# Performance work log

Hardware: AMD Instinct MI355X
Metric: run time of the kernel (lower is better)

## Reference

```python
import jax, jax.numpy as jnp
import numpy as np

GROUPS = 8
EPS = 1e-3  # keras GroupNormalization default epsilon


def group_norm(x, gamma, beta):
    # x: [B,H,W,C], groups over channel axis
    B, H, W, C = x.shape
    g = GROUPS
    xr = x.reshape(B, H, W, g, C // g)
    mean = jnp.mean(xr, axis=(1, 2, 4), keepdims=True)
    var = jnp.var(xr, axis=(1, 2, 4), keepdims=True)
    xn = (xr - mean) * jax.lax.rsqrt(var + EPS)
    xn = xn.reshape(B, H, W, C)
    return xn * gamma + beta


def setup_inputs() -> dict:
    key = jax.random.key(0)
    ks = jax.random.split(key, 6)
    B, H, W, C = 8, 64, 64, 64
    std = 0.02
    return {
        "x": jax.random.normal(ks[0], (B, H, W, C), dtype=jnp.float32),
        "gamma": jnp.ones((C,), dtype=jnp.float32),
        "beta": jnp.zeros((C,), dtype=jnp.float32),
        "wq": jax.random.normal(ks[1], (C, C), dtype=jnp.float32) * std,
        "bq": jnp.zeros((C,), dtype=jnp.float32),
        "wk": jax.random.normal(ks[2], (C, C), dtype=jnp.float32) * std,
        "bk": jnp.zeros((C,), dtype=jnp.float32),
        "wv": jax.random.normal(ks[3], (C, C), dtype=jnp.float32) * std,
        "bv": jnp.zeros((C,), dtype=jnp.float32),
        "wp": jax.random.normal(ks[4], (C, C), dtype=jnp.float32) * std,
        "bp": jnp.zeros((C,), dtype=jnp.float32),
    }


def reference(x, gamma, beta, wq, bq, wk, bk, wv, bv, wp, bp):
    B, H, W, C = x.shape
    scale = jnp.asarray(C, x.dtype) ** -0.5
    h = group_norm(x, gamma, beta)  # note: residual uses normalized input (as in source)
    q = h @ wq + bq
    k = h @ wk + bk
    v = h @ wv + bv
    # full O((HW)^2) score tensor, exactly as the original
    attn = jnp.einsum('bhwc,bHWc->bhwHW', q, k) * scale
    attn = jax.nn.softmax(attn.reshape(B, H, W, H * W), axis=-1)
    attn = attn.reshape(B, H, W, H, W)
    proj = jnp.einsum('bhwHW,bHWc->bhwc', attn, v)
    proj = proj @ wp + bp
    return h + proj
```

## Files before the change

### kernel.cpp

```cpp
#include <hip/hip_runtime.h>

#define NTOK 4096
#define CH 64
#define LOG2E 1.4426950408889634f

typedef __bf16 bf8 __attribute__((ext_vector_type(8)));
typedef __bf16 bf4 __attribute__((ext_vector_type(4)));
typedef _Float16 h8 __attribute__((ext_vector_type(8)));
typedef _Float16 h4 __attribute__((ext_vector_type(4)));
typedef float f4 __attribute__((ext_vector_type(4)));

__device__ __forceinline__ f4 mfma16(bf8 a, bf8 b, f4 c) {
    return __builtin_amdgcn_mfma_f32_16x16x32_bf16(a, b, c, 0, 0, 0);
}
__device__ __forceinline__ f4 mfma32h(h8 a, h8 b, f4 c) {
    return __builtin_amdgcn_mfma_f32_16x16x32_f16(a, b, c, 0, 0, 0);
}

__global__ __launch_bounds__(256) void pre_kernel(const float* __restrict__ wq,
                                                  const float* __restrict__ wk,
                                                  const float* __restrict__ wv,
                                                  const float* __restrict__ wp,
                                                  const float* __restrict__ x,
                                                  __bf16* __restrict__ wqt,
                                                  __bf16* __restrict__ wkt,
                                                  __bf16* __restrict__ wvt,
                                                  __bf16* __restrict__ wpt,
                                                  float* __restrict__ gpart) {
    int t = threadIdx.x;
    if (blockIdx.x < 4) {
        int m = blockIdx.x;
        const float* src = (m == 0) ? wq : (m == 1) ? wk : (m == 2) ? wv : wp;
        __bf16* dst      = (m == 0) ? wqt : (m == 1) ? wkt : (m == 2) ? wvt : wpt;
        __shared__ float s[64][65];
        for (int i = 0; i < 16; ++i) {
            int e = i * 256 + t;
            s[e >> 6][e & 63] = src[e];
        }
        __syncthreads();
        int o = t >> 2, seg = t & 3;
        for (int j = 0; j < 16; ++j) {
            int in = seg * 16 + j;
            dst[o * 64 + in] = (__bf16)s[in][o];
        }
        return;
    }
    int bid = blockIdx.x - 4;
    int b = bid >> 6, slab = bid & 63;
    const float4* xb = (const float4*)(x + (size_t)(b * NTOK + slab * 64) * CH);
    float s = 0.f, ss = 0.f;
    for (int i = 0; i < 4; ++i) {
        int row = (t >> 4) + i * 16;
        float4 v = xb[row * 16 + (t & 15)];
        s  += v.x + v.y + v.z + v.w;
        ss += v.x * v.x + v.y * v.y + v.z * v.z + v.w * v.w;
    }
    __shared__ float ls[256], lss[256];
    ls[t] = s; lss[t] = ss;
    __syncthreads();
    if (t < 8) {
        float a = 0.f, aa = 0.f;
        for (int p = 0; p < 16; ++p) {
            a  += ls[p * 16 + 2 * t]  + ls[p * 16 + 2 * t + 1];
            aa += lss[p * 16 + 2 * t] + lss[p * 16 + 2 * t + 1];
        }
        gpart[((b * 64 + slab) * 8 + t) * 2 + 0] = a;
        gpart[((b * 64 + slab) * 8 + t) * 2 + 1] = aa;
    }
}

__global__ __launch_bounds__(256) void qkv_gn(const float* __restrict__ x,
                                              const float* __restrict__ gpart,
                                              const float* __restrict__ gamma,
                                              const float* __restrict__ beta,
                                              const __bf16* __restrict__ wqt,
                                              const __bf16* __restrict__ wkt,
                                              const __bf16* __restrict__ wvt,
                                              const float* __restrict__ bq,
                                              const float* __restrict__ bk,
                                              const float* __restrict__ bv,
                                              __bf16* __restrict__ q,
                                              __bf16* __restrict__ k,
                                              _Float16* __restrict__ vT) {
    __shared__ __bf16 W[3][64][72];
    __shared__ __bf16 Hl[64][72];
    __shared__ _Float16 Vst[64][68];
    __shared__ float red[128];
    __shared__ float sstat[16];
    int t = threadIdx.x;
    size_t rowbase = (size_t)blockIdx.x * 64;
    int b = (int)(rowbase >> 12), tokbase = (int)(rowbase & 4095);
    if (t < 64) {
        int gi = t & 7, c = t >> 3;
        const float2* gp = (const float2*)gpart + (size_t)b * 512 + gi;
        float a = 0.f, aa = 0.f;
        for (int p = c * 8; p < c * 8 + 8; ++p) {
            float2 v = gp[(size_t)p * 8];
            a += v.x; aa += v.y;
        }
        red[t * 2] = a; red[t * 2 + 1] = aa;
    }
    for (int m = 0; m < 3; ++m) {
        const __bf16* src = (m == 0) ? wqt : (m == 1) ? wkt : wvt;
        for (int i = 0; i < 2; ++i) {
            int e = i * 256 + t, row = e >> 3, ch = e & 7;
            *(bf8*)&W[m][row][ch * 8] = *(const bf8*)(src + row * 64 + ch * 8);
        }
    }
    __syncthreads();
    if (t < 8) {
        float a = 0.f, aa = 0.f;
        for (int c = 0; c < 8; ++c) {
            a  += red[(c * 8 + t) * 2];
            aa += red[(c * 8 + t) * 2 + 1];
        }
        float mean = a * (1.f / 32768.f);
        float var = aa * (1.f / 32768.f) - mean * mean;
        sstat[t * 2 + 0] = mean;
        sstat[t * 2 + 1] = rsqrtf(var + 1e-3f);
    }
    __syncthreads();
    {
        int c4 = (t & 15) * 4, grp = c4 >> 3;
        float mean = sstat[grp * 2], rstd = sstat[grp * 2 + 1];
        float g0 = gamma[c4] * rstd, g1 = gamma[c4 + 1] * rstd,
              g2 = gamma[c4 + 2] * rstd, g3 = gamma[c4 + 3] * rstd;
        float b0 = beta[c4], b1 = beta[c4 + 1], b2 = beta[c4 + 2], b3 = beta[c4 + 3];
        const float4* xb = (const float4*)(x + rowbase * 64);
        for (int i = 0; i < 4; ++i) {
            int row = (t >> 4) + i * 16;
            float4 v = xb[row * 16 + (t & 15)];
            bf4 hv;
            hv[0] = (__bf16)((v.x - mean) * g0 + b0);
            hv[1] = (__bf16)((v.y - mean) * g1 + b1);
            hv[2] = (__bf16)((v.z - mean) * g2 + b2);
            hv[3] = (__bf16)((v.w - mean) * g3 + b3);
            *(bf4*)&Hl[row][c4] = hv;
        }
    }
    __syncthreads();
    int lane = t & 63, wave = t >> 6, quad = lane >> 4, l15 = lane & 15;
    bf8 a0 = *(const bf8*)&Hl[wave * 16 + l15][quad * 8];
    bf8 a1 = *(const bf8*)&Hl[wave * 16 + l15][32 + quad * 8];
    for (int m = 0; m < 3; ++m) {
        const float* bias = (m == 0) ? bq : (m == 1) ? bk : bv;
        float sc = (m == 0) ? 0.125f * LOG2E : 1.0f;
        for (int tt = 0; tt < 4; ++tt) {
            int col = l15 + 16 * tt;
            bf8 b0 = *(const bf8*)&W[m][col][quad * 8];
            bf8 b1 = *(const bf8*)&W[m][col][32 + quad * 8];
            f4 acc = {0.f, 0.f, 0.f, 0.f};
            acc = mfma16(a0, b0, acc);
            acc = mfma16(a1, b1, acc);
            float bb = bias[col];
            if (m == 2) {
                for (int r = 0; r < 4; ++r)
                    Vst[col][wave * 16 + quad * 4 + r] = (_Float16)(acc[r] + bb);
            } else {
                __bf16* dst = (m == 0) ? q : k;
                for (int r = 0; r < 4; ++r) {
                    float val = (acc[r] + bb) * sc;
                    dst[(rowbase + wave * 16 + quad * 4 + r) * 64 + col] = (__bf16)val;
                }
            }
        }
    }
    __syncthreads();
    {
        int d = wave * 16 + l15;
        for (int kb = 0; kb < 2; ++kb) {
            h4 lo = *(const h4*)&Vst[d][kb * 32 + quad * 4];
            h4 hi = *(const h4*)&Vst[d][kb * 32 + 16 + quad * 4];
            h8 o;
            o[0] = lo[0]; o[1] = lo[1]; o[2] = lo[2]; o[3] = lo[3];
            o[4] = hi[0]; o[5] = hi[1]; o[6] = hi[2]; o[7] = hi[3];
            _Float16* dst = vT + ((((size_t)b * 128 + (tokbase >> 5) + kb) * 4 + wave) * 64
                                  + lane) * 8;
            *(h8*)dst = o;
        }
    }
}

__global__ __launch_bounds__(256, 2) void attn_final(const __bf16* __restrict__ q,
                                                     const __bf16* __restrict__ k,
                                                     const _Float16* __restrict__ vt,
                                                     const __bf16* __restrict__ wpt,
                                                     const float* __restrict__ bp,
                                                     const float* __restrict__ x,
                                                     const float* __restrict__ gpart,
                                                     const float* __restrict__ gamma,
                                                     const float* __restrict__ beta,
                                                     float* __restrict__ out) {
    __shared__ _Float16 Om[2][64][72];
    __shared__ float sS[2][64];
    __shared__ __bf16 Wl[64][72];
    __shared__ __bf16 Ol[64][72];
    __shared__ float red[128];
    __shared__ float sstat[16], sg[64], sb[64];

    int bid = blockIdx.x;
    int qt = bid >> 3, b = bid & 7;
    int t = threadIdx.x, lane = t & 63, w = t >> 6, quad = lane >> 4, l15 = lane & 15;

    for (int i = 0; i < 2; ++i) {
        int e = i * 256 + t, row = e >> 3, ch = e & 7;
        *(bf8*)&Wl[row][ch * 8] = *(const bf8*)(wpt + row * 64 + ch * 8);
    }
    if (t < 64) { sg[t] = gamma[t]; sb[t] = beta[t]; }
    if (t < 64) {
        int gi = t & 7, c = t >> 3;
        const float2* gp = (const float2*)gpart + (size_t)b * 512 + gi;
        float a = 0.f, aa = 0.f;
        for (int p = c * 8; p < c * 8 + 8; ++p) {
            float2 v = gp[(size_t)p * 8];
            a += v.x; aa += v.y;
        }
        red[t * 2] = a; red[t * 2 + 1] = aa;
    }

    const __bf16* qbase = q + ((size_t)b * NTOK + qt * 64) * 64;
    bf8 aq[4][2];
    for (int s = 0; s < 4; ++s) {
        const __bf16* r = qbase + (s * 16 + l15) * 64;
        aq[s][0] = *(const bf8*)(r + quad * 8);
        aq[s][1] = *(const bf8*)(r + 32 + quad * 8);
    }
    const __bf16* kbase   = k  + ((size_t)b * NTOK + w * 1024) * 64;
    const _Float16* vbase = vt + (size_t)b * 262144 + (size_t)(w * 32) * 2048 + lane * 8;

    f4 acc[4][4] = {};
    float li[4] = {0.f, 0.f, 0.f, 0.f};

    for (int it = 0; it < 32; ++it) {
        const __bf16* kr0 = kbase + (size_t)(it * 32 + l15) * 64;
        const __bf16* kr1 = kr0 + 16 * 64;
        bf8 kf00 = *(const bf8*)(kr0 + quad * 8);
        bf8 kf01 = *(const bf8*)(kr0 + 32 + quad * 8);
        bf8 kf10 = *(const bf8*)(kr1 + quad * 8);
        bf8 kf11 = *(const bf8*)(kr1 + 32 + quad * 8);
        const _Float16* vr = vbase + (size_t)it * 2048;
        h8 vf0 = *(const h8*)(vr);
        h8 vf1 = *(const h8*)(vr + 512);
        h8 vf2 = *(const h8*)(vr + 1024);
        h8 vf3 = *(const h8*)(vr + 1536);

        for (int s = 0; s < 4; ++s) {
            f4 St0 = {0.f, 0.f, 0.f, 0.f};
            f4 St1 = {0.f, 0.f, 0.f, 0.f};
            St0 = mfma16(kf00, aq[s][0], St0);
            St0 = mfma16(kf01, aq[s][1], St0);
            St1 = mfma16(kf10, aq[s][0], St1);
            St1 = mfma16(kf11, aq[s][1], St1);
            h8 pf;
            float rs = 0.f;
            for (int r = 0; r < 4; ++r) {
                float p0 = __builtin_amdgcn_exp2f(St0[r]);
                float p1 = __builtin_amdgcn_exp2f(St1[r]);
                rs += p0 + p1;
                pf[r]     = (_Float16)p0;
                pf[4 + r] = (_Float16)p1;
            }
            li[s] += rs;
            acc[s][0] = mfma32h(vf0, pf, acc[s][0]);
            acc[s][1] = mfma32h(vf1, pf, acc[s][1]);
            acc[s][2] = mfma32h(vf2, pf, acc[s][2]);
            acc[s][3] = mfma32h(vf3, pf, acc[s][3]);
        }
    }

    for (int s = 0; s < 4; ++s) {
        li[s] += __shfl_xor(li[s], 16);
        li[s] += __shfl_xor(li[s], 32);
    }

    if (w >= 2) {
        for (int s = 0; s < 4; ++s) {
            for (int td = 0; td < 4; ++td) {
                h4 o4;
                for (int r = 0; r < 4; ++r) o4[r] = (_Float16)acc[s][td][r];
                *(h4*)&Om[w - 2][s * 16 + l15][td * 16 + quad * 4] = o4;
            }
            if (quad == 0) sS[w - 2][s * 16 + l15] = li[s];
        }
    }
    __syncthreads();
    if (t < 8) {
        float a = 0.f, aa = 0.f;
        for (int c = 0; c < 8; ++c) {
            a  += red[(c * 8 + t) * 2];
            aa += red[(c * 8 + t) * 2 + 1];
        }
        float mean = a * (1.f / 32768.f);
        float var = aa * (1.f / 32768.f) - mean * mean;
        sstat[t * 2 + 0] = mean;
        sstat[t * 2 + 1] = rsqrtf(var + 1e-3f);
    }
    if (w < 2) {
        for (int s = 0; s < 4; ++s) {
            for (int td = 0; td < 4; ++td) {
                h4 o4 = *(const h4*)&Om[w][s * 16 + l15][td * 16 + quad * 4];
                for (int r = 0; r < 4; ++r) acc[s][td][r] += (float)o4[r];
            }
            li[s] += sS[w][s * 16 + l15];
        }
    }
    __syncthreads();
    if (w < 2) {
        for (int s = 0; s < 4; ++s) {
            for (int td = 0; td < 4; ++td) {
                h4 o4;
                for (int r = 0; r < 4; ++r) o4[r] = (_Float16)acc[s][td][r];
                *(h4*)&Om[w][s * 16 + l15][td * 16 + quad * 4] = o4;
            }
            if (quad == 0) sS[w][s * 16 + l15] = li[s];
        }
    }
    __syncthreads();
    {
        int qq = t >> 2, ds = (t & 3) * 16;
        float inv = 1.f / (sS[0][qq] + sS[1][qq]);
        h8 a0 = *(const h8*)&Om[0][qq][ds];
        h8 b0 = *(const h8*)&Om[0][qq][ds + 8];
        h8 a1 = *(const h8*)&Om[1][qq][ds];
        h8 b1 = *(const h8*)&Om[1][qq][ds + 8];
        bf8 olo, ohi;
        for (int j = 0; j < 8; ++j) {
            olo[j] = (__bf16)(((float)a0[j] + (float)a1[j]) * inv);
            ohi[j] = (__bf16)(((float)b0[j] + (float)b1[j]) * inv);
        }
        *(bf8*)&Ol[qq][ds] = olo;
        *(bf8*)&Ol[qq][ds + 8] = ohi;
    }
    __syncthreads();
    size_t rowbase = ((size_t)b * NTOK + qt * 64) + w * 16;
    bf8 a0 = *(const bf8*)&Ol[w * 16 + l15][quad * 8];
    bf8 a1 = *(const bf8*)&Ol[w * 16 + l15][32 + quad * 8];
    for (int tt = 0; tt < 4; ++tt) {
        int col = l15 + 16 * tt;
        bf8 b0 = *(const bf8*)&Wl[col][quad * 8];
        bf8 b1 = *(const bf8*)&Wl[col][32 + quad * 8];
        f4 pacc = {0.f, 0.f, 0.f, 0.f};
        pacc = mfma16(a0, b0, pacc);
        pacc = mfma16(a1, b1, pacc);
        int grp = col >> 3;
        float mean = sstat[grp * 2], gs = sg[col] * sstat[grp * 2 + 1], bs = sb[col];
        float bias = bp[col];
        for (int r = 0; r < 4; ++r) {
            size_t gi = (rowbase + quad * 4 + r) * 64 + col;
            float h = (x[gi] - mean) * gs + bs;
            out[gi] = pacc[r] + bias + h;
        }
    }
}

extern "C" void kernel_launch(void* const* d_in, const int* in_sizes, int n_in,
                              void* d_out, int out_size, void* d_ws, size_t ws_size,
                              hipStream_t stream) {
    const float* x     = (const float*)d_in[0];
    const float* gamma = (const float*)d_in[1];
    const float* beta  = (const float*)d_in[2];
    const float* wq    = (const float*)d_in[3];
    const float* bq    = (const float*)d_in[4];
    const float* wk    = (const float*)d_in[5];
    const float* bk    = (const float*)d_in[6];
    const float* wv    = (const float*)d_in[7];
    const float* bv    = (const float*)d_in[8];
    const float* wp    = (const float*)d_in[9];
    const float* bp    = (const float*)d_in[10];
    float* out = (float*)d_out;

    char* ws = (char*)d_ws;
    const size_t MB = 1024 * 1024;
    __bf16*   qb   = (__bf16*)(ws);
    __bf16*   kb   = (__bf16*)(ws + 4 * MB);
    _Float16* vtb  = (_Float16*)(ws + 8 * MB);
    __bf16*   wqt  = (__bf16*)(ws + 12 * MB);
    __bf16*   wkt  = (__bf16*)(ws + 12 * MB + 8192);
    __bf16*   wvt  = (__bf16*)(ws + 12 * MB + 16384);
    __bf16*   wpt  = (__bf16*)(ws + 12 * MB + 24576);
    float*    gpart = (float*)(ws + 12 * MB + 32768);

    pre_kernel<<<516, 256, 0, stream>>>(wq, wk, wv, wp, x, wqt, wkt, wvt, wpt, gpart);
    qkv_gn<<<512, 256, 0, stream>>>(x, gpart, gamma, beta, wqt, wkt, wvt, bq, bk, bv, qb, kb, vtb);
    attn_final<<<512, 256, 0, stream>>>(qb, kb, vtb, wpt, bp, x, gpart, gamma, beta, out);
}
```

Measured before the change: 133.5 us.

## Double-buffer K/V register loads and compute softmax row sums via MFMA

The attention inner loop is restructured to prefetch the next K/V tile into a second register set while the current one is computed, with s_setprio raised around the compute sections. Row sums of exp values are now accumulated by an extra MFMA against a vector of ones, replacing scalar adds and cross-lane shuffles. Exp results are packed to fp16 with cvt_pkrtz. This aims to hide global load latency and cut VALU work, at the cost of higher register pressure, an extra MFMA per step, and round-toward-zero fp16 rounding in the row sum.

Result: no change. 134.5 us (+0.8%).

```diff
diff --git a/kernel.cpp b/kernel.cpp
--- a/kernel.cpp
+++ b/kernel.cpp
@@ -8,6 +8,7 @@
 typedef __bf16 bf4 __attribute__((ext_vector_type(4)));
 typedef _Float16 h8 __attribute__((ext_vector_type(8)));
 typedef _Float16 h4 __attribute__((ext_vector_type(4)));
+typedef __fp16 fp16x2 __attribute__((ext_vector_type(2)));
 typedef float f4 __attribute__((ext_vector_type(4)));
 
 __device__ __forceinline__ f4 mfma16(bf8 a, bf8 b, f4 c) {
@@ -181,6 +182,50 @@
     }
 }
 
+__device__ __forceinline__ void load_kv(const __bf16* kr0, const _Float16* vr, int quad,
+                                        bf8 kf[4], h8 vf[4]) {
+    kf[0] = *(const bf8*)(kr0 + quad * 8);
+    kf[1] = *(const bf8*)(kr0 + 32 + quad * 8);
+    kf[2] = *(const bf8*)(kr0 + 1024 + quad * 8);
+    kf[3] = *(const bf8*)(kr0 + 1024 + 32 + quad * 8);
+    vf[0] = *(const h8*)(vr);
+    vf[1] = *(const h8*)(vr + 512);
+    vf[2] = *(const h8*)(vr + 1024);
+    vf[3] = *(const h8*)(vr + 1536);
+}
+
+__device__ __forceinline__ void compute32(const bf8 kf[4], const h8 vf[4],
+                                          const bf8 aq[4][2], h8 ones,
+                                          f4 acc[4][4], f4 acc_li[4]) {
+#pragma unroll
+    for (int s = 0; s < 4; ++s) {
+        f4 St0 = {0.f, 0.f, 0.f, 0.f};
+        f4 St1 = {0.f, 0.f, 0.f, 0.f};
+        St0 = mfma16(kf[0], aq[s][0], St0);
+        St0 = mfma16(kf[1], aq[s][1], St0);
+        St1 = mfma16(kf[2], aq[s][0], St1);
+        St1 = mfma16(kf[3], aq[s][1], St1);
+        float p00 = __builtin_amdgcn_exp2f(St0[0]);
+        float p01 = __builtin_amdgcn_exp2f(St0[1]);
+        float p02 = __builtin_amdgcn_exp2f(St0[2]);
+        float p03 = __builtin_amdgcn_exp2f(St0[3]);
+        float p10 = __builtin_amdgcn_exp2f(St1[0]);
+        float p11 = __builtin_amdgcn_exp2f(St1[1]);
+        float p12 = __builtin_amdgcn_exp2f(St1[2]);
+        float p13 = __builtin_amdgcn_exp2f(St1[3]);
+        h8 pf;
+        ((fp16x2*)&pf)[0] = __builtin_amdgcn_cvt_pkrtz(p00, p01);
+        ((fp16x2*)&pf)[1] = __builtin_amdgcn_cvt_pkrtz(p02, p03);
+        ((fp16x2*)&pf)[2] = __builtin_amdgcn_cvt_pkrtz(p10, p11);
+        ((fp16x2*)&pf)[3] = __builtin_amdgcn_cvt_pkrtz(p12, p13);
+        acc_li[s] = mfma32h(ones, pf, acc_li[s]);
+        acc[s][0] = mfma32h(vf[0], pf, acc[s][0]);
+        acc[s][1] = mfma32h(vf[1], pf, acc[s][1]);
+        acc[s][2] = mfma32h(vf[2], pf, acc[s][2]);
+        acc[s][3] = mfma32h(vf[3], pf, acc[s][3]);
+    }
+}
+
 __global__ __launch_bounds__(256, 2) void attn_final(const __bf16* __restrict__ q,
                                                      const __bf16* __restrict__ k,
                                                      const _Float16* __restrict__ vt,
@@ -228,50 +273,33 @@
     const __bf16* kbase   = k  + ((size_t)b * NTOK + w * 1024) * 64;
     const _Float16* vbase = vt + (size_t)b * 262144 + (size_t)(w * 32) * 2048 + lane * 8;
 
+    h8 ones;
+#pragma unroll
+    for (int j = 0; j < 8; ++j) ones[j] = (_Float16)1.f;
+
     f4 acc[4][4] = {};
-    float li[4] = {0.f, 0.f, 0.f, 0.f};
-
-    for (int it = 0; it < 32; ++it) {
-        const __bf16* kr0 = kbase + (size_t)(it * 32 + l15) * 64;
-        const __bf16* kr1 = kr0 + 16 * 64;
-        bf8 kf00 = *(const bf8*)(kr0 + quad * 8);
-        bf8 kf01 = *(const bf8*)(kr0 + 32 + quad * 8);
-        bf8 kf10 = *(const bf8*)(kr1 + quad * 8);
-        bf8 kf11 = *(const bf8*)(kr1 + 32 + quad * 8);
-        const _Float16* vr = vbase + (size_t)it * 2048;
-        h8 vf0 = *(const h8*)(vr);
-        h8 vf1 = *(const h8*)(vr + 512);
-        h8 vf2 = *(const h8*)(vr + 1024);
-        h8 vf3 = *(const h8*)(vr + 1536);
-
-        for (int s = 0; s < 4; ++s) {
-            f4 St0 = {0.f, 0.f, 0.f, 0.f};
-            f4 St1 = {0.f, 0.f, 0.f, 0.f};
-            St0 = mfma16(kf00, aq[s][0], St0);
-            St0 = mfma16(kf01, aq[s][1], St0);
-            St1 = mfma16(kf10, aq[s][0], St1);
-            St1 = mfma16(kf11, aq[s][1], St1);
-            h8 pf;
-            float rs = 0.f;
-            for (int r = 0; r < 4; ++r) {
-                float p0 = __builtin_amdgcn_exp2f(St0[r]);
-                float p1 = __builtin_amdgcn_exp2f(St1[r]);
-                rs += p0 + p1;
-                pf[r]     = (_Float16)p0;
-                pf[4 + r] = (_Float16)p1;
-            }
-            li[s] += rs;
-            acc[s][0] = mfma32h(vf0, pf, acc[s][0]);
-            acc[s][1] = mfma32h(vf1, pf, acc[s][1]);
-            acc[s][2] = mfma32h(vf2, pf, acc[s][2]);
-            acc[s][3] = mfma32h(vf3, pf, acc[s][3]);
-        }
-    }
-
-    for (int s = 0; s < 4; ++s) {
-        li[s] += __shfl_xor(li[s], 16);
-        li[s] += __shfl_xor(li[s], 32);
-    }
+    f4 acc_li[4] = {};
+
+    bf8 kfA[4], kfB[4];
+    h8 vfA[4], vfB[4];
+    load_kv(kbase + (size_t)l15 * 64, vbase, quad, kfA, vfA);
+    for (int it = 0; it < 32; it += 2) {
+        load_kv(kbase + (size_t)((it + 1) * 32 + l15) * 64,
+                vbase + (size_t)(it + 1) * 2048, quad, kfB, vfB);
+        __builtin_amdgcn_s_setprio(1);
+        compute32(kfA, vfA, aq, ones, acc, acc_li);
+        __builtin_amdgcn_s_setprio(0);
+        if (it + 2 < 32)
+            load_kv(kbase + (size_t)((it + 2) * 32 + l15) * 64,
+                    vbase + (size_t)(it + 2) * 2048, quad, kfA, vfA);
+        __builtin_amdgcn_s_setprio(1);
+        compute32(kfB, vfB, aq, ones, acc, acc_li);
+        __builtin_amdgcn_s_setprio(0);
+    }
+
+    float li[4];
+#pragma unroll
+    for (int s = 0; s < 4; ++s) li[s] = acc_li[s][0];
 
     if (w >= 2) {
         for (int s = 0; s < 4; ++s) {
```
